# Kernel optimization log

Hardware: AMD Instinct MI355X
Metric: run time of the kernel (lower is better)

The kernel has to match this reference:

```python
import jax, jax.numpy as jnp
import numpy as np

NH = 8
DIM = 512
NP = 1024
MNP = 4096
BS = 4
TOPK = 32


def setup_inputs() -> dict:
    key = jax.random.key(0)
    ks = jax.random.split(key, 10)
    q = jax.random.normal(ks[0], (NP, BS, DIM), dtype=jnp.float32)
    k = jax.random.normal(ks[1], (MNP, BS, DIM), dtype=jnp.float32)
    v = jax.random.normal(ks[2], (MNP, BS, DIM), dtype=jnp.float32)
    rns_indices = jax.random.randint(ks[3], (BS, NP, TOPK), 0, MNP)
    s = 0.02
    W1 = jax.random.normal(ks[4], (DIM, DIM), dtype=jnp.float32) * s
    b1 = jnp.zeros((DIM,), dtype=jnp.float32)
    W2 = jax.random.normal(ks[5], (DIM, DIM), dtype=jnp.float32) * s
    b2 = jnp.zeros((DIM,), dtype=jnp.float32)
    W3 = jax.random.normal(ks[6], (DIM, DIM), dtype=jnp.float32) * s
    b3 = jnp.zeros((DIM,), dtype=jnp.float32)
    return {"q": q, "k": k, "v": v, "rns_indices": rns_indices,
            "W1": W1, "b1": b1, "W2": W2, "b2": b2, "W3": W3, "b3": b3}


def reference(q, k, v, rns_indices, W1, b1, W2, b2, W3, b3):
    np_, bs, dim = q.shape
    mnp = k.shape[0]
    nh = NH
    dh = dim // nh
    # seq-first -> batch-first, linear projections (torch Linear: x @ W.T + b)
    qh = (jnp.einsum('nbd,ed->bne', q, W1) + b1).reshape(bs, np_, nh, dh)
    kh = (jnp.einsum('mbd,ed->bme', k, W2) + b2).reshape(bs, mnp, nh, dh)
    vh = (jnp.einsum('mbd,ed->bme', v, W3) + b3).reshape(bs, mnp, nh, dh)
    # dense scores: [bs, nh, np, mnp]
    w = jnp.einsum('bnhd,bmhd->bhnm', qh, kh) / jnp.sqrt(jnp.asarray(dh, w_dtype := qh.dtype))
    # scatter-built neighbor mask: [bs, np, mnp] (shared across heads)
    b_idx = jnp.arange(bs)[:, None, None]
    n_idx = jnp.arange(np_)[None, :, None]
    mask = jnp.zeros((bs, np_, mnp), dtype=w.dtype).at[b_idx, n_idx, rns_indices].set(1.0)
    mask = mask[:, None, :, :]  # broadcast over heads
    w = w * mask + (-1e9) * (1.0 - mask)
    w = jax.nn.softmax(w, axis=3)
    out = jnp.einsum('bhnm,bmhd->nbhd', w, vh).reshape(np_, bs, dim)
    return out
```

## Files before the change

kernel.cpp:

```cpp
#include <hip/hip_runtime.h>
#include <stdint.h>

#define NH   8
#define DIM  512
#define NP   1024
#define MNP  4096
#define BS   4
#define TOPK 32
#define DH   64

typedef unsigned short u16;
typedef __attribute__((ext_vector_type(8))) short bf16x8;
typedef __attribute__((ext_vector_type(4))) float f32x4;

__device__ __forceinline__ u16 f2bf(float f) {
    union { float f; unsigned u; } x; x.f = f;
    unsigned r = x.u + 0x7FFFu + ((x.u >> 16) & 1u);
    return (u16)(r >> 16);
}
__device__ __forceinline__ float bf2f(u16 h) {
    union { unsigned u; float f; } x; x.u = ((unsigned)h) << 16;
    return x.f;
}

__device__ __forceinline__ void async16(const void* g, void* l) {
    __builtin_amdgcn_global_load_lds(
        (const __attribute__((address_space(1))) unsigned int*)g,
        (__attribute__((address_space(3))) unsigned int*)l, 16, 0, 0);
}

__global__ void cvt_all(const float* __restrict__ W1, const float* __restrict__ W2,
                        const float* __restrict__ W3, const float* __restrict__ q,
                        const float* __restrict__ k,  const float* __restrict__ v,
                        u16* __restrict__ wall, u16* __restrict__ act) {
    const size_t base = ((size_t)blockIdx.x * 256 + threadIdx.x) * 4;
    const size_t gstride = (size_t)4800 * 256 * 4;
#pragma unroll
    for (int g = 0; g < 4; g++) {
        size_t i = base + (size_t)g * gstride;
        const float* s; u16* d;
        if (i < 786432) {
            d = wall + i;
            s = (i < 262144) ? W1 + i : (i < 524288) ? W2 + (i - 262144) : W3 + (i - 524288);
        } else {
            size_t j = i - 786432;
            d = act + j;
            s = (j < 2097152) ? q + j : (j < 10485760) ? k + (j - 2097152) : v + (j - 10485760);
        }
        float4 val = *(const float4*)s;
        ushort4 o;
        o.x = f2bf(val.x); o.y = f2bf(val.y); o.z = f2bf(val.z); o.w = f2bf(val.w);
        *(ushort4*)d = o;
    }
}

__global__ __launch_bounds__(256, 2)
void proj_gemm(const u16* __restrict__ act, const u16* __restrict__ wall,
               const float* __restrict__ b1, const float* __restrict__ b2,
               const float* __restrict__ b3, u16* __restrict__ outall) {
    __shared__ u16 As[2][128 * 64];
    __shared__ u16 Bs[2][128 * 64];

    const int bid = blockIdx.x;
    const int x = bid / 288;
    const int t = bid % 288;
    int z, y;
    if (t < 32)       { z = 0; y = t; }
    else if (t < 160) { z = 1; y = t - 32; }
    else              { z = 2; y = t - 160; }

    const size_t aoff = (z == 0) ? 0u : (z == 1) ? 2097152u : 10485760u;
    const u16* A = act + aoff;
    const u16* W = wall + (size_t)z * 262144;
    const float* bias = (z == 0) ? b1 : (z == 1) ? b2 : b3;
    u16* C = outall + aoff;

    const int tid  = threadIdx.x;
    const int bm   = y * 128;
    const int bn   = x * 128;
    const int wave = tid >> 6;
    const int lane = tid & 63;
    const int wm   = (wave & 1) * 64;
    const int wn   = (wave >> 1) * 64;
    const int l16  = lane & 15;
    const int quad = lane >> 4;

    const int srow = lane >> 3;
    const int scol = ((lane & 7) ^ srow) * 8;

    const int lrow = wave * 32;
    const u16* Ag = A + (size_t)(bm + lrow + srow) * 512 + scol;
    const u16* Wg = W + (size_t)(bn + lrow + srow) * 512 + scol;

    f32x4 acc[4][4] = {};

    #define STAGE(buf, k0)                                                     \
        _Pragma("unroll")                                                      \
        for (int r = 0; r < 4; r++) {                                          \
            async16(Ag + (size_t)(r * 8) * 512 + (k0),                         \
                    &As[buf][(lrow + r * 8) * 64 + lane * 8]);                 \
            async16(Wg + (size_t)(r * 8) * 512 + (k0),                         \
                    &Bs[buf][(lrow + r * 8) * 64 + lane * 8]);                 \
        }

    STAGE(0, 0);

#pragma unroll
    for (int kt = 0; kt < 8; kt++) {
        const int cur = kt & 1;
        if (kt < 7) {
            STAGE(cur ^ 1, (kt + 1) * 64);
            asm volatile("s_waitcnt vmcnt(8)" ::: "memory");
        } else {
            asm volatile("s_waitcnt vmcnt(0)" ::: "memory");
        }
        __builtin_amdgcn_s_barrier();
#pragma unroll
        for (int kk = 0; kk < 64; kk += 32) {
            bf16x8 af[4], bfr[4];
            const int g = (kk >> 3) + quad;
#pragma unroll
            for (int i = 0; i < 4; i++) {
                int ra = wm + i * 16 + l16;
                int rb = wn + i * 16 + l16;
                af[i]  = *(const bf16x8*)(&As[cur][ra * 64 + ((g ^ (ra & 7)) << 3)]);
                bfr[i] = *(const bf16x8*)(&Bs[cur][rb * 64 + ((g ^ (rb & 7)) << 3)]);
            }
#pragma unroll
            for (int i = 0; i < 4; i++)
#pragma unroll
                for (int j = 0; j < 4; j++)
                    acc[i][j] = __builtin_amdgcn_mfma_f32_16x16x32_bf16(
                        af[i], bfr[j], acc[i][j], 0, 0, 0);
        }
        __builtin_amdgcn_s_barrier();
    }
    #undef STAGE

#pragma unroll
    for (int i = 0; i < 4; i++) {
        int row = bm + wm + i * 16 + quad * 4;
#pragma unroll
        for (int j = 0; j < 4; j++) {
            int col = bn + wn + j * 16 + l16;
            float bv = bias[col];
#pragma unroll
            for (int r = 0; r < 4; r++)
                C[(size_t)(row + r) * 512 + col] = f2bf(acc[i][j][r] + bv);
        }
    }
}

__global__ __launch_bounds__(256)
void attn_kernel(const u16* __restrict__ Qh, const u16* __restrict__ Kh,
                 const u16* __restrict__ Vh, const int* __restrict__ rns,
                 float* __restrict__ out) {
    __shared__ float sq[4][512];
    __shared__ float swt[4][32 * 9];
    __shared__ int   srw[4][TOPK];

    const int wv   = threadIdx.x >> 6;
    const int lane = threadIdx.x & 63;
    const int pair = blockIdx.x * 4 + wv;
    const int n = pair >> 2;
    const int b = pair & 3;
    const int s   = lane >> 1;
    const int sub = lane & 1;

    int myidx = rns[(b * NP + n) * TOPK + s];
    int myrow = (myidx * BS + b) * DIM;
    if (sub == 0) srw[wv][s] = myrow;

    bool dup = false;
#pragma unroll
    for (int j = 0; j < TOPK; j++) {
        int other = __shfl(myidx, j * 2, 64);
        dup = dup || ((j < s) && (other == myidx));
    }

    {
        const u16* qrow = Qh + (size_t)pair * DIM;
        uint4 qv = *(const uint4*)(qrow + lane * 8);
        float4 f0 = { bf2f((u16)qv.x), bf2f((u16)(qv.x >> 16)),
                      bf2f((u16)qv.y), bf2f((u16)(qv.y >> 16)) };
        float4 f1 = { bf2f((u16)qv.z), bf2f((u16)(qv.z >> 16)),
                      bf2f((u16)qv.w), bf2f((u16)(qv.w >> 16)) };
        *(float4*)(&sq[wv][lane * 8])     = f0;
        *(float4*)(&sq[wv][lane * 8 + 4]) = f1;
    }
    __builtin_amdgcn_wave_barrier();

    const float* qw = sq[wv];
    float sc[NH];
#pragma unroll
    for (int h = 0; h < NH; h++) {
        const u16* kp = Kh + myrow + h * DH + sub * 32;
        const float* qp = qw + h * DH + sub * 32;
        float acc = 0.f;
#pragma unroll
        for (int d = 0; d < 32; d += 8) {
            uint4 kv = *(const uint4*)(kp + d);
            acc += qp[d + 0] * bf2f((u16)kv.x) + qp[d + 1] * bf2f((u16)(kv.x >> 16))
                 + qp[d + 2] * bf2f((u16)kv.y) + qp[d + 3] * bf2f((u16)(kv.y >> 16))
                 + qp[d + 4] * bf2f((u16)kv.z) + qp[d + 5] * bf2f((u16)(kv.z >> 16))
                 + qp[d + 6] * bf2f((u16)kv.w) + qp[d + 7] * bf2f((u16)(kv.w >> 16));
        }
        sc[h] = acc;
    }
#pragma unroll
    for (int h = 0; h < NH; h++) {
        sc[h] += __shfl_xor(sc[h], 1, 64);
        sc[h] = dup ? -1e30f : sc[h] * 0.125f;
    }
    float w[NH];
#pragma unroll
    for (int h = 0; h < NH; h++) {
        float m = sc[h];
        m = fmaxf(m, __shfl_xor(m, 2, 64));
        m = fmaxf(m, __shfl_xor(m, 4, 64));
        m = fmaxf(m, __shfl_xor(m, 8, 64));
        m = fmaxf(m, __shfl_xor(m, 16, 64));
        m = fmaxf(m, __shfl_xor(m, 32, 64));
        float e = __expf(sc[h] - m);
        float t = e;
        t += __shfl_xor(t, 2, 64);
        t += __shfl_xor(t, 4, 64);
        t += __shfl_xor(t, 8, 64);
        t += __shfl_xor(t, 16, 64);
        t += __shfl_xor(t, 32, 64);
        w[h] = e / t;
    }
    if (sub == 0) {
#pragma unroll
        for (int h = 0; h < NH; h++) swt[wv][s * 9 + h] = w[h];
    }
    __builtin_amdgcn_wave_barrier();

    const int h  = lane >> 3;
    const int e8 = lane * 8;
    float a[8] = {0, 0, 0, 0, 0, 0, 0, 0};
#pragma unroll 8
    for (int si = 0; si < TOPK; si++) {
        int   row = srw[wv][si];
        float wgt = swt[wv][si * 9 + h];
        uint4 vv = *(const uint4*)(Vh + row + e8);
        a[0] += wgt * bf2f((u16)vv.x); a[1] += wgt * bf2f((u16)(vv.x >> 16));
        a[2] += wgt * bf2f((u16)vv.y); a[3] += wgt * bf2f((u16)(vv.y >> 16));
        a[4] += wgt * bf2f((u16)vv.z); a[5] += wgt * bf2f((u16)(vv.z >> 16));
        a[6] += wgt * bf2f((u16)vv.w); a[7] += wgt * bf2f((u16)(vv.w >> 16));
    }
    float* op = out + (size_t)pair * DIM + e8;
    float4 o0 = {a[0], a[1], a[2], a[3]};
    float4 o1 = {a[4], a[5], a[6], a[7]};
    *(float4*)op       = o0;
    *((float4*)op + 1) = o1;
}

extern "C" void kernel_launch(void* const* d_in, const int* in_sizes, int n_in,
                              void* d_out, int out_size, void* d_ws, size_t ws_size,
                              hipStream_t stream) {
    const float* q  = (const float*)d_in[0];
    const float* k  = (const float*)d_in[1];
    const float* v  = (const float*)d_in[2];
    const int* rns  = (const int*)d_in[3];
    const float* W1 = (const float*)d_in[4];
    const float* b1 = (const float*)d_in[5];
    const float* W2 = (const float*)d_in[6];
    const float* b2 = (const float*)d_in[7];
    const float* W3 = (const float*)d_in[8];
    const float* b3 = (const float*)d_in[9];
    float* out = (float*)d_out;

    u16* ws   = (u16*)d_ws;
    u16* wall = ws;
    u16* act  = wall + 786432;
    u16* proj = act + 18874368;
    u16* Qh = proj;
    u16* Kh = proj + 2097152;
    u16* Vh = proj + 10485760;

    cvt_all<<<4800, 256, 0, stream>>>(W1, W2, W3, q, k, v, wall, act);
    proj_gemm<<<1152, 256, 0, stream>>>(act, wall, b1, b2, b3, proj);
    attn_kernel<<<NP * BS / 4, 256, 0, stream>>>(Qh, Kh, Vh, rns, out);
}
```

Measured before the change: 187.0 us.

## Retile projection GEMM to 256x128 blocks with 512 threads and BK=32

```diff
diff --git a/kernel.cpp b/kernel.cpp
--- a/kernel.cpp
+++ b/kernel.cpp
@@ -54,20 +54,20 @@
     }
 }
 
-__global__ __launch_bounds__(256, 2)
+__global__ __launch_bounds__(512, 6)
 void proj_gemm(const u16* __restrict__ act, const u16* __restrict__ wall,
                const float* __restrict__ b1, const float* __restrict__ b2,
                const float* __restrict__ b3, u16* __restrict__ outall) {
     __shared__ u16 As[2][128 * 64];
-    __shared__ u16 Bs[2][128 * 64];
+    __shared__ u16 Bs[2][64 * 64];
 
     const int bid = blockIdx.x;
-    const int x = bid / 288;
-    const int t = bid % 288;
+    const int x = bid / 144;
+    const int t = bid % 144;
     int z, y;
-    if (t < 32)       { z = 0; y = t; }
-    else if (t < 160) { z = 1; y = t - 32; }
-    else              { z = 2; y = t - 160; }
+    if (t < 16)      { z = 0; y = t; }
+    else if (t < 80) { z = 1; y = t - 16; }
+    else             { z = 2; y = t - 80; }
 
     const size_t aoff = (z == 0) ? 0u : (z == 1) ? 2097152u : 10485760u;
     const u16* A = act + aoff;
@@ -76,55 +76,56 @@
     u16* C = outall + aoff;
 
     const int tid  = threadIdx.x;
-    const int bm   = y * 128;
+    const int bm   = y * 256;
     const int bn   = x * 128;
     const int wave = tid >> 6;
     const int lane = tid & 63;
-    const int wm   = (wave & 1) * 64;
-    const int wn   = (wave >> 1) * 64;
+    const int wm   = (wave & 3) * 64;
+    const int wn   = (wave >> 2) * 64;
     const int l16  = lane & 15;
     const int quad = lane >> 4;
 
-    const int srow = lane >> 3;
-    const int scol = ((lane & 7) ^ srow) * 8;
-
-    const int lrow = wave * 32;
-    const u16* Ag = A + (size_t)(bm + lrow + srow) * 512 + scol;
-    const u16* Wg = W + (size_t)(bn + lrow + srow) * 512 + scol;
+    const int pA   = tid >> 3;
+    const int q3   = tid & 7;
+    const int posA = q3 ^ (pA & 7);
+    const int hA   = posA >> 2;
+    const int gA   = posA & 3;
+    const int rA   = 2 * pA + hA;
+    const u16* Asrc = A + (size_t)(bm + rA) * 512 + gA * 8;
+    const u16* Bsrc = W + (size_t)(bn + rA) * 512 + gA * 8;
 
     f32x4 acc[4][4] = {};
 
     #define STAGE(buf, k0)                                                     \
-        _Pragma("unroll")                                                      \
-        for (int r = 0; r < 4; r++) {                                          \
-            async16(Ag + (size_t)(r * 8) * 512 + (k0),                         \
-                    &As[buf][(lrow + r * 8) * 64 + lane * 8]);                 \
-            async16(Wg + (size_t)(r * 8) * 512 + (k0),                         \
-                    &Bs[buf][(lrow + r * 8) * 64 + lane * 8]);                 \
-        }
+        async16(Asrc + (k0),               &As[buf][tid * 8]);                 \
+        async16(Asrc + 128 * 512 + (k0),   &As[buf][tid * 8 + 4096]);          \
+        async16(Bsrc + (k0),               &Bs[buf][tid * 8]);
 
     STAGE(0, 0);
 
 #pragma unroll
-    for (int kt = 0; kt < 8; kt++) {
+    for (int kt = 0; kt < 16; kt++) {
         const int cur = kt & 1;
-        if (kt < 7) {
-            STAGE(cur ^ 1, (kt + 1) * 64);
-            asm volatile("s_waitcnt vmcnt(8)" ::: "memory");
+        if (kt < 15) {
+            STAGE(cur ^ 1, (kt + 1) * 32);
+            asm volatile("s_waitcnt vmcnt(3)" ::: "memory");
         } else {
             asm volatile("s_waitcnt vmcnt(0)" ::: "memory");
         }
         __builtin_amdgcn_s_barrier();
-#pragma unroll
-        for (int kk = 0; kk < 64; kk += 32) {
+        {
             bf16x8 af[4], bfr[4];
-            const int g = (kk >> 3) + quad;
 #pragma unroll
             for (int i = 0; i < 4; i++) {
                 int ra = wm + i * 16 + l16;
-                int rb = wn + i * 16 + l16;
-                af[i]  = *(const bf16x8*)(&As[cur][ra * 64 + ((g ^ (ra & 7)) << 3)]);
-                bfr[i] = *(const bf16x8*)(&Bs[cur][rb * 64 + ((g ^ (rb & 7)) << 3)]);
+                af[i] = *(const bf16x8*)(&As[cur][(ra >> 1) * 64 +
+                          (((((ra & 1) << 2) | quad) ^ ((ra >> 1) & 7)) << 3)]);
+            }
+#pragma unroll
+            for (int j = 0; j < 4; j++) {
+                int rb = wn + j * 16 + l16;
+                bfr[j] = *(const bf16x8*)(&Bs[cur][(rb >> 1) * 64 +
+                          (((((rb & 1) << 2) | quad) ^ ((rb >> 1) & 7)) << 3)]);
             }
 #pragma unroll
             for (int i = 0; i < 4; i++)
@@ -280,6 +281,6 @@
     u16* Vh = proj + 10485760;
 
     cvt_all<<<4800, 256, 0, stream>>>(W1, W2, W3, q, k, v, wall, act);
-    proj_gemm<<<1152, 256, 0, stream>>>(act, wall, b1, b2, b3, proj);
+    proj_gemm<<<576, 512, 0, stream>>>(act, wall, b1, b2, b3, proj);
     attn_kernel<<<NP * BS / 4, 256, 0, stream>>>(Qh, Kh, Vh, rns, out);
 }
```

Measured after the change: 372.3 us. 1.99x slower.
